# Optimization experiments

Measured on AMD Instinct MI355X. Metric: run time of the kernel, lower is better.

The kernel has to match this reference:

```python
import jax, jax.numpy as jnp
import numpy as np

B, N, D = 4, 2048, 1024
H = 16
HD = D // H


def setup_inputs() -> dict:
    key = jax.random.key(0)
    ks = jax.random.split(key, 7)
    bound_w = 1.0 / np.sqrt(D)  # kaiming_uniform(a=sqrt(5)) on (D, D) -> U(-1/sqrt(fan_in), 1/sqrt(fan_in))
    x = jax.random.normal(ks[0], (B, N, D), dtype=jnp.float32)
    Wq = jax.random.uniform(ks[1], (D, D), jnp.float32, -bound_w, bound_w)
    Wk = jax.random.uniform(ks[2], (D, D), jnp.float32, -bound_w, bound_w)
    Wv = jax.random.uniform(ks[3], (D, D), jnp.float32, -bound_w, bound_w)
    Wo = jax.random.uniform(ks[4], (D, D), jnp.float32, -bound_w, bound_w)
    bo = jax.random.uniform(ks[5], (D,), jnp.float32, -bound_w, bound_w)
    return {"x": x, "Wq": Wq, "Wk": Wk, "Wv": Wv, "Wo": Wo, "bo": bo}


def reference(x, Wq, Wk, Wv, Wo, bo):
    b, n, _ = x.shape
    # QKV projections: contraction over W's FIRST axis, matching torch einsum 'bnd,di->bni'
    Q = jnp.einsum('bnd,di->bni', x, Wq)
    K = jnp.einsum('bnd,di->bni', x, Wk)
    V = jnp.einsum('bnd,di->bni', x, Wv)
    # split heads: [b, h, n, hd]
    Q = Q.reshape(b, n, H, HD).transpose(0, 2, 1, 3)
    K = K.reshape(b, n, H, HD).transpose(0, 2, 1, 3)
    V = V.reshape(b, n, H, HD).transpose(0, 2, 1, 3)
    scores = jnp.einsum('bhnd,bhmd->bhnm', Q, K) / np.sqrt(HD).astype(np.float32)
    causal = jnp.triu(jnp.ones((n, n), dtype=bool), k=1)  # True above diagonal -> masked
    scores = jnp.where(causal[None, None, :, :], -jnp.inf, scores)
    attn = jax.nn.softmax(scores, axis=-1)
    # dropout rate is 0.0 -> identity
    ctx = jnp.einsum('bhnm,bhmd->bhnd', attn, V)
    ctx = ctx.transpose(0, 2, 1, 3).reshape(b, n, D)
    return ctx @ Wo.T + bo
```

## Files before the change

kernel.cpp:

```cpp
#include <hip/hip_runtime.h>
#include <hip/hip_bf16.h>

typedef __bf16 bf16;
typedef __bf16 bf16x4 __attribute__((ext_vector_type(4)));
typedef __bf16 bf16x8 __attribute__((ext_vector_type(8)));
typedef float  f32x4  __attribute__((ext_vector_type(4)));

#define B_  4
#define N_  2048
#define D_  1024
#define H_  16
#define HD_ 64

#define QSCALE 0.1803368801111204f

__device__ __forceinline__ bf16x8 ld8(const bf16* p) {
  return *reinterpret_cast<const bf16x8*>(p);
}
__device__ __forceinline__ float max3f(float a, float b, float c) {
  return fmaxf(fmaxf(a, b), c);
}

__device__ __forceinline__ void gload16(const bf16* g, bf16* l) {
  __builtin_amdgcn_global_load_lds(
      (const __attribute__((address_space(1))) void*)g,
      (__attribute__((address_space(3))) void*)l, 16, 0, 0);
}

__global__ __launch_bounds__(256) void cast_k(const float* __restrict__ in,
                                              bf16* __restrict__ out, int n) {
  int i = (blockIdx.x * 256 + threadIdx.x) * 8;
  if (i >= n) return;
  float4 a = *reinterpret_cast<const float4*>(in + i);
  float4 b = *reinterpret_cast<const float4*>(in + i + 4);
  bf16x8 o;
  o[0] = (bf16)a.x; o[1] = (bf16)a.y; o[2] = (bf16)a.z; o[3] = (bf16)a.w;
  o[4] = (bf16)b.x; o[5] = (bf16)b.y; o[6] = (bf16)b.z; o[7] = (bf16)b.w;
  *reinterpret_cast<bf16x8*>(out + i) = o;
}

__global__ __launch_bounds__(1024)
void transpose3_k(const float* __restrict__ w0, const float* __restrict__ w1,
                  const float* __restrict__ w2, bf16* __restrict__ out) {
  __shared__ float t[32][33];
  const int z = blockIdx.z;
  const float* in = (z == 0) ? w0 : (z == 1) ? w1 : w2;
  const float scale = (z == 0) ? QSCALE : 1.0f;
  bf16* o = out + (size_t)z * D_ * D_;
  int c = blockIdx.x * 32 + threadIdx.x;
  int r = blockIdx.y * 32 + threadIdx.y;
  t[threadIdx.y][threadIdx.x] = in[r * D_ + c];
  __syncthreads();
  int oc = blockIdx.y * 32 + threadIdx.x;
  int orr = blockIdx.x * 32 + threadIdx.y;
  o[orr * D_ + oc] = (bf16)(scale * t[threadIdx.x][threadIdx.y]);
}

#define GEMM_CORE(A_, Bt_, K_)                                                   \
  f32x4 acc[4][4] = {};                                                          \
  for (int kk = 0; kk < (K_); kk += 32) {                                        \
    _Pragma("unroll")                                                            \
    for (int j = 0; j < 2; ++j) {                                                \
      gload16(&(A_)[(size_t)(brow + wid * 32 + j * 16 + (lane >> 2)) * (K_) +    \
                    kk + (lane & 3) * 8],                                        \
              &As[(wid * 32 + j * 16) * 32]);                                    \
      gload16(&(Bt_)[(size_t)(bcol + wid * 32 + j * 16 + (lane >> 2)) * (K_) +   \
                     kk + (lane & 3) * 8],                                       \
              &Bs[(wid * 32 + j * 16) * 32]);                                    \
    }                                                                            \
    __syncthreads();                                                             \
    bf16x8 af[4], bfr[4];                                                        \
    _Pragma("unroll")                                                            \
    for (int m = 0; m < 4; ++m)                                                  \
      af[m] = *reinterpret_cast<const bf16x8*>(&As[(wr + m * 16 + l15) * 32 + lk]); \
    _Pragma("unroll")                                                            \
    for (int n = 0; n < 4; ++n)                                                  \
      bfr[n] = *reinterpret_cast<const bf16x8*>(&Bs[(wc + n * 16 + l15) * 32 + lk]); \
    _Pragma("unroll")                                                            \
    for (int m = 0; m < 4; ++m)                                                  \
      _Pragma("unroll")                                                          \
      for (int n = 0; n < 4; ++n)                                                \
        acc[m][n] = __builtin_amdgcn_mfma_f32_16x16x32_bf16(af[m], bfr[n],       \
                                                            acc[m][n], 0, 0, 0); \
    __syncthreads();                                                             \
  }

__global__ __launch_bounds__(256)
void gemm_qkv(const bf16* __restrict__ A, const bf16* __restrict__ Bt,
              bf16* __restrict__ qb, bf16* __restrict__ kb, bf16* __restrict__ vtb)
{
  __shared__ bf16 As[128 * 32];
  __shared__ bf16 Bs[128 * 32];
  const int tid  = threadIdx.x;
  const int lane = tid & 63;
  const int wid  = tid >> 6;
  const int wg   = blockIdx.x;
  const int xcd  = wg & 7;
  const int idx  = wg >> 3;
  const int brow = ((xcd << 3) + (idx & 7)) * 128;
  const int bcol = (idx >> 3) * 128;
  const int wr   = (wid >> 1) * 64;
  const int wc   = (wid & 1) * 64;
  const int l15  = lane & 15;
  const int lk   = (lane >> 4) * 8;

  GEMM_CORE(A, Bt, D_)

  const int which = bcol >> 10;
  bf16* outp = (which == 0) ? qb : (which == 1) ? kb : vtb;
  const int r0 = (lane >> 4) * 4;
#pragma unroll
  for (int m = 0; m < 4; ++m)
#pragma unroll
    for (int n = 0; n < 4; ++n)
#pragma unroll
      for (int r = 0; r < 4; ++r) {
        int grow = brow + wr + m * 16 + r0 + r;
        int gcol = (bcol & 1023) + wc + n * 16 + l15;
        int b = grow >> 11, nn = grow & (N_ - 1);
        int h = gcol >> 6, hd = gcol & 63;
        float v = acc[m][n][r];
        if (which == 2)
          outp[((size_t)((b * H_ + h) * HD_ + hd)) * N_ + nn] = (bf16)v;
        else
          outp[((((size_t)(b * H_ + h)) * N_ + nn) << 6) + hd] = (bf16)v;
      }
}

__global__ __launch_bounds__(256)
void gemm_out(const bf16* __restrict__ A, const bf16* __restrict__ Bt,
              float* __restrict__ C, const float* __restrict__ bias)
{
  __shared__ bf16 As[128 * 32];
  __shared__ bf16 Bs[128 * 32];
  const int tid  = threadIdx.x;
  const int lane = tid & 63;
  const int wid  = tid >> 6;
  const int wg   = blockIdx.x;
  const int xcd  = wg & 7;
  const int idx  = wg >> 3;
  const int brow = ((xcd << 3) + (idx & 7)) * 128;
  const int bcol = (idx >> 3) * 128;
  const int wr   = (wid >> 1) * 64;
  const int wc   = (wid & 1) * 64;
  const int l15  = lane & 15;
  const int lk   = (lane >> 4) * 8;

  GEMM_CORE(A, Bt, D_)

  const int r0 = (lane >> 4) * 4;
#pragma unroll
  for (int m = 0; m < 4; ++m)
#pragma unroll
    for (int n = 0; n < 4; ++n)
#pragma unroll
      for (int r = 0; r < 4; ++r) {
        int grow = brow + wr + m * 16 + r0 + r;
        int gcol = bcol + wc + n * 16 + l15;
        C[(size_t)grow * D_ + gcol] = acc[m][n][r] + bias[gcol];
      }
}

__global__ __launch_bounds__(512, 6)
void attn_k(const bf16* __restrict__ q, const bf16* __restrict__ k,
            const bf16* __restrict__ vt, bf16* __restrict__ ctx)
{
  __shared__ bf16 Ks[2][64 * 64];
  __shared__ bf16 Vs[2][64 * 64];
  __shared__ bf16 Pl[8][16][72];
  const int tid  = threadIdx.x;
  const int lane = tid & 63;
  const int wid  = tid >> 6;
  const int bid  = blockIdx.x;
  const int bh   = bid & 63;
  const int cpr  = bid >> 6;
  const int l15  = lane & 15;
  const int g    = lane >> 4;
  const int lk   = g * 8;
  const int swz  = (l15 & 7) << 4;

  const bf16* kp = k  + (size_t)bh * N_ * HD_;
  const bf16* vp = vt + (size_t)bh * HD_ * N_;
  const int b = bh >> 4, h = bh & 15;

  const int srow  = wid * 8 + (lane >> 3);
  const int scoff = ((lane & 7) ^ (srow & 7)) * 8;
  const int sdoff = wid * 8 * 64;

  bf16x8 ones8;
#pragma unroll
  for (int i = 0; i < 8; ++i) ones8[i] = (bf16)1.0f;

#pragma unroll
  for (int p = 0; p < 2; ++p) {
    const int qb0   = (p == 0 ? cpr : 15 - cpr) * 128;
    const int qbase = qb0 + wid * 16;
    const int nt    = qb0 / 64 + 2;
    const int tm    = qbase >> 6;

    const bf16* qp = q + ((size_t)bh * N_ + qbase) * HD_;
    bf16x8 aq[2];
#pragma unroll
    for (int c2 = 0; c2 < 2; ++c2)
      aq[c2] = ld8(qp + (size_t)l15 * HD_ + c2 * 32 + lk);

    float m_run = -1e30f;
    f32x4 oacc[5] = {};

    gload16(kp + (size_t)srow * HD_ + scoff, &Ks[0][sdoff]);
    gload16(vp + (size_t)srow * N_ + scoff, &Vs[0][sdoff]);
    __syncthreads();

    for (int t = 0; t < nt; ++t) {
      const int cur = t & 1;
      if (t + 1 < nt) {
        const int kb = (t + 1) * 64;
        gload16(kp + (size_t)(kb + srow) * HD_ + scoff, &Ks[cur ^ 1][sdoff]);
        gload16(vp + (size_t)srow * N_ + kb + scoff, &Vs[cur ^ 1][sdoff]);
      }
      if (t <= tm) {
        const char* kb_ = (const char*)&Ks[cur][0];
        const char* vb_ = (const char*)&Vs[cur][0];

        f32x4 s[4] = {};
#pragma unroll
        for (int tt = 0; tt < 4; ++tt) {
          bf16x8 bk0 = *reinterpret_cast<const bf16x8*>(
              kb_ + (tt * 16 + l15) * 128 + ((g * 16) ^ swz));
          bf16x8 bk1 = *reinterpret_cast<const bf16x8*>(
              kb_ + (tt * 16 + l15) * 128 + ((64 + g * 16) ^ swz));
          s[tt] = __builtin_amdgcn_mfma_f32_16x16x32_bf16(bk0, aq[0], s[tt], 0, 0, 0);
          s[tt] = __builtin_amdgcn_mfma_f32_16x16x32_bf16(bk1, aq[1], s[tt], 0, 0, 0);
        }

        if (t == tm) {
          const int qr = qbase + l15;
#pragma unroll
          for (int tt = 0; tt < 4; ++tt)
#pragma unroll
            for (int r = 0; r < 4; ++r) {
              int kq = t * 64 + tt * 16 + g * 4 + r;
              if (kq > qr) s[tt][r] = -1e30f;
            }
        }

        float pm = max3f(s[0][0], s[0][1], s[0][2]);
        pm = max3f(pm, s[0][3], s[1][0]);
        pm = max3f(pm, s[1][1], s[1][2]);
        pm = max3f(pm, s[1][3], s[2][0]);
        pm = max3f(pm, s[2][1], s[2][2]);
        pm = max3f(pm, s[2][3], s[3][0]);
        pm = max3f(pm, s[3][1], s[3][2]);
        pm = fmaxf(pm, s[3][3]);
        pm = fmaxf(pm, __shfl_xor(pm, 16));
        pm = fmaxf(pm, __shfl_xor(pm, 32));
        if (!__all(pm <= m_run + 8.f)) {
          float mn = fmaxf(m_run, pm);
          float al = exp2f(m_run - mn);
          m_run = mn;
#pragma unroll
          for (int n = 0; n < 5; ++n)
#pragma unroll
            for (int r = 0; r < 4; ++r) oacc[n][r] *= al;
        }
#pragma unroll
        for (int tt = 0; tt < 4; ++tt)
#pragma unroll
          for (int r = 0; r < 4; ++r) s[tt][r] = exp2f(s[tt][r] - m_run);

#pragma unroll
        for (int tt = 0; tt < 4; ++tt) {
          bf16x4 pk;
#pragma unroll
          for (int r = 0; r < 4; ++r) pk[r] = (bf16)s[tt][r];
          *reinterpret_cast<bf16x4*>(&Pl[wid][l15][tt * 16 + g * 4]) = pk;
        }

#pragma unroll
        for (int kc = 0; kc < 2; ++kc) {
          bf16x8 pb = *reinterpret_cast<const bf16x8*>(&Pl[wid][l15][kc * 32 + lk]);
#pragma unroll
          for (int n = 0; n < 4; ++n) {
            bf16x8 vf = *reinterpret_cast<const bf16x8*>(
                vb_ + (n * 16 + l15) * 128 + ((kc * 64 + g * 16) ^ swz));
            oacc[n] = __builtin_amdgcn_mfma_f32_16x16x32_bf16(vf, pb, oacc[n], 0, 0, 0);
          }
          oacc[4] = __builtin_amdgcn_mfma_f32_16x16x32_bf16(ones8, pb, oacc[4], 0, 0, 0);
        }
      }
      __syncthreads();
    }

    float inv = 1.f / oacc[4][0];
    bf16* cp = ctx + ((size_t)b * N_ + qbase + l15) * D_ + h * HD_;
#pragma unroll
    for (int n = 0; n < 4; ++n) {
      bf16x4 o;
#pragma unroll
      for (int r = 0; r < 4; ++r) o[r] = (bf16)(oacc[n][r] * inv);
      *reinterpret_cast<bf16x4*>(cp + n * 16 + g * 4) = o;
    }
  }
}

extern "C" void kernel_launch(void* const* d_in, const int* in_sizes, int n_in,
                              void* d_out, int out_size, void* d_ws, size_t ws_size,
                              hipStream_t stream)
{
  const float* x  = (const float*)d_in[0];
  const float* Wq = (const float*)d_in[1];
  const float* Wk = (const float*)d_in[2];
  const float* Wv = (const float*)d_in[3];
  const float* Wo = (const float*)d_in[4];
  const float* bo = (const float*)d_in[5];
  float* out = (float*)d_out;

  const size_t SZ_BHND = (size_t)B_ * H_ * N_ * HD_ * sizeof(bf16);
  const size_t SZ_W    = (size_t)D_ * D_ * sizeof(bf16);
  char* ws = (char*)d_ws;
  bf16* xbf  = (bf16*)(ws);
  bf16* ctx  = (bf16*)(ws);
  bf16* qb   = (bf16*)(ws + SZ_BHND);
  bf16* kbf  = (bf16*)(ws + 2 * SZ_BHND);
  bf16* vtb  = (bf16*)(ws + 3 * SZ_BHND);
  bf16* wqkv = (bf16*)(ws + 4 * SZ_BHND);
  bf16* wob  = (bf16*)(ws + 4 * SZ_BHND + 3 * SZ_W);
  if (ws_size < 4 * SZ_BHND + 4 * SZ_W) return;

  const int NX = B_ * N_ * D_;
  cast_k<<<NX / (256 * 8), 256, 0, stream>>>(x, xbf, NX);
  cast_k<<<(D_ * D_) / (256 * 8), 256, 0, stream>>>(Wo, wob, D_ * D_);

  transpose3_k<<<dim3(32, 32, 3), dim3(32, 32), 0, stream>>>(Wq, Wk, Wv, wqkv);

  gemm_qkv<<<1536, 256, 0, stream>>>(xbf, wqkv, qb, kbf, vtb);

  attn_k<<<512, 512, 0, stream>>>(qb, kbf, vtb, ctx);

  gemm_out<<<512, 256, 0, stream>>>(ctx, wob, out, bo);
}
```

Measured before the change: 195.1 us.

## Deepen GEMM K-tile with swizzled LDS; split attention into 64-row blocks

The GEMM core now stages 64-wide K tiles with an XOR-swizzled LDS layout, which halves the number of barriers and is meant to avoid LDS bank conflicts. The attention kernel drops the paired 128-row causal blocks of 8 waves and instead launches 2048 blocks of 4 waves, each handling 64 query rows, ordered longest-first. This removes the idle waves that skipped tiles past their diagonal and gives finer load balancing. In exchange, each K/V tile is reused by fewer waves, so K/V loads are amortized over less work, and LDS use per GEMM block doubles.

```diff
diff --git a/kernel.cpp b/kernel.cpp
--- a/kernel.cpp
+++ b/kernel.cpp
@@ -56,41 +56,47 @@
   o[orr * D_ + oc] = (bf16)(scale * t[threadIdx.x][threadIdx.y]);
 }
 
-#define GEMM_CORE(A_, Bt_, K_)                                                   \
-  f32x4 acc[4][4] = {};                                                          \
-  for (int kk = 0; kk < (K_); kk += 32) {                                        \
-    _Pragma("unroll")                                                            \
-    for (int j = 0; j < 2; ++j) {                                                \
-      gload16(&(A_)[(size_t)(brow + wid * 32 + j * 16 + (lane >> 2)) * (K_) +    \
-                    kk + (lane & 3) * 8],                                        \
-              &As[(wid * 32 + j * 16) * 32]);                                    \
-      gload16(&(Bt_)[(size_t)(bcol + wid * 32 + j * 16 + (lane >> 2)) * (K_) +   \
-                     kk + (lane & 3) * 8],                                       \
-              &Bs[(wid * 32 + j * 16) * 32]);                                    \
-    }                                                                            \
-    __syncthreads();                                                             \
-    bf16x8 af[4], bfr[4];                                                        \
-    _Pragma("unroll")                                                            \
-    for (int m = 0; m < 4; ++m)                                                  \
-      af[m] = *reinterpret_cast<const bf16x8*>(&As[(wr + m * 16 + l15) * 32 + lk]); \
-    _Pragma("unroll")                                                            \
-    for (int n = 0; n < 4; ++n)                                                  \
-      bfr[n] = *reinterpret_cast<const bf16x8*>(&Bs[(wc + n * 16 + l15) * 32 + lk]); \
-    _Pragma("unroll")                                                            \
-    for (int m = 0; m < 4; ++m)                                                  \
-      _Pragma("unroll")                                                          \
-      for (int n = 0; n < 4; ++n)                                                \
-        acc[m][n] = __builtin_amdgcn_mfma_f32_16x16x32_bf16(af[m], bfr[n],       \
-                                                            acc[m][n], 0, 0, 0); \
-    __syncthreads();                                                             \
+#define GEMM_CORE(A_, Bt_, K_)                                                    \
+  f32x4 acc[4][4] = {};                                                           \
+  const int sr8   = lane >> 3;                           \
+  const int schk  = ((lane & 7) ^ sr8) * 8;         \
+  const int swz7  = (l15 & 7);                                                    \
+  for (int kk = 0; kk < (K_); kk += 64) {                                         \
+    _Pragma("unroll")                                                             \
+    for (int j = 0; j < 4; ++j) {                                                 \
+      const int rr = j * 32 + wid * 8 + sr8;                                      \
+      gload16(&(A_)[(size_t)(brow + rr) * (K_) + kk + schk],                      \
+              &As[(j * 32 + wid * 8) * 64]);                                      \
+      gload16(&(Bt_)[(size_t)(bcol + rr) * (K_) + kk + schk],                     \
+              &Bs[(j * 32 + wid * 8) * 64]);                                      \
+    }                                                                             \
+    __syncthreads();                                                              \
+    _Pragma("unroll")                                                             \
+    for (int s = 0; s < 2; ++s) {                                                 \
+      const int q = ((s * 4 + g) ^ swz7) * 8;                                     \
+      bf16x8 af[4], bfr[4];                                                       \
+      _Pragma("unroll")                                                           \
+      for (int m = 0; m < 4; ++m)                                                 \
+        af[m] = *reinterpret_cast<const bf16x8*>(&As[(wr + m * 16 + l15) * 64 + q]); \
+      _Pragma("unroll")                                                           \
+      for (int n = 0; n < 4; ++n)                                                 \
+        bfr[n] = *reinterpret_cast<const bf16x8*>(&Bs[(wc + n * 16 + l15) * 64 + q]); \
+      _Pragma("unroll")                                                           \
+      for (int m = 0; m < 4; ++m)                                                 \
+        _Pragma("unroll")                                                         \
+        for (int n = 0; n < 4; ++n)                                               \
+          acc[m][n] = __builtin_amdgcn_mfma_f32_16x16x32_bf16(af[m], bfr[n],      \
+                                                              acc[m][n], 0, 0, 0);\
+    }                                                                             \
+    __syncthreads();                                                              \
   }
 
 __global__ __launch_bounds__(256)
 void gemm_qkv(const bf16* __restrict__ A, const bf16* __restrict__ Bt,
               bf16* __restrict__ qb, bf16* __restrict__ kb, bf16* __restrict__ vtb)
 {
-  __shared__ bf16 As[128 * 32];
-  __shared__ bf16 Bs[128 * 32];
+  __shared__ bf16 As[128 * 64];
+  __shared__ bf16 Bs[128 * 64];
   const int tid  = threadIdx.x;
   const int lane = tid & 63;
   const int wid  = tid >> 6;
@@ -102,13 +108,13 @@
   const int wr   = (wid >> 1) * 64;
   const int wc   = (wid & 1) * 64;
   const int l15  = lane & 15;
-  const int lk   = (lane >> 4) * 8;
+  const int g    = lane >> 4;
 
   GEMM_CORE(A, Bt, D_)
 
   const int which = bcol >> 10;
   bf16* outp = (which == 0) ? qb : (which == 1) ? kb : vtb;
-  const int r0 = (lane >> 4) * 4;
+  const int r0 = g * 4;
 #pragma unroll
   for (int m = 0; m < 4; ++m)
 #pragma unroll
@@ -131,8 +137,8 @@
 void gemm_out(const bf16* __restrict__ A, const bf16* __restrict__ Bt,
               float* __restrict__ C, const float* __restrict__ bias)
 {
-  __shared__ bf16 As[128 * 32];
-  __shared__ bf16 Bs[128 * 32];
+  __shared__ bf16 As[128 * 64];
+  __shared__ bf16 Bs[128 * 64];
   const int tid  = threadIdx.x;
   const int lane = tid & 63;
   const int wid  = tid >> 6;
@@ -144,11 +150,11 @@
   const int wr   = (wid >> 1) * 64;
   const int wc   = (wid & 1) * 64;
   const int l15  = lane & 15;
-  const int lk   = (lane >> 4) * 8;
+  const int g    = lane >> 4;
 
   GEMM_CORE(A, Bt, D_)
 
-  const int r0 = (lane >> 4) * 4;
+  const int r0 = g * 4;
 #pragma unroll
   for (int m = 0; m < 4; ++m)
 #pragma unroll
@@ -161,19 +167,19 @@
       }
 }
 
-__global__ __launch_bounds__(512, 6)
+__global__ __launch_bounds__(256, 3)
 void attn_k(const bf16* __restrict__ q, const bf16* __restrict__ k,
             const bf16* __restrict__ vt, bf16* __restrict__ ctx)
 {
   __shared__ bf16 Ks[2][64 * 64];
   __shared__ bf16 Vs[2][64 * 64];
-  __shared__ bf16 Pl[8][16][72];
+  __shared__ bf16 Pl[4][16][72];
   const int tid  = threadIdx.x;
   const int lane = tid & 63;
   const int wid  = tid >> 6;
   const int bid  = blockIdx.x;
   const int bh   = bid & 63;
-  const int cpr  = bid >> 6;
+  const int c    = 31 - (bid >> 6);
   const int l15  = lane & 15;
   const int g    = lane >> 4;
   const int lk   = g * 8;
@@ -183,123 +189,127 @@
   const bf16* vp = vt + (size_t)bh * HD_ * N_;
   const int b = bh >> 4, h = bh & 15;
 
-  const int srow  = wid * 8 + (lane >> 3);
-  const int scoff = ((lane & 7) ^ (srow & 7)) * 8;
-  const int sdoff = wid * 8 * 64;
+  const int sr8   = lane >> 3;
+  const int scoff = ((lane & 7) ^ sr8) * 8;
 
   bf16x8 ones8;
 #pragma unroll
   for (int i = 0; i < 8; ++i) ones8[i] = (bf16)1.0f;
 
-#pragma unroll
-  for (int p = 0; p < 2; ++p) {
-    const int qb0   = (p == 0 ? cpr : 15 - cpr) * 128;
-    const int qbase = qb0 + wid * 16;
-    const int nt    = qb0 / 64 + 2;
-    const int tm    = qbase >> 6;
-
-    const bf16* qp = q + ((size_t)bh * N_ + qbase) * HD_;
-    bf16x8 aq[2];
-#pragma unroll
-    for (int c2 = 0; c2 < 2; ++c2)
-      aq[c2] = ld8(qp + (size_t)l15 * HD_ + c2 * 32 + lk);
-
-    float m_run = -1e30f;
-    f32x4 oacc[5] = {};
-
-    gload16(kp + (size_t)srow * HD_ + scoff, &Ks[0][sdoff]);
-    gload16(vp + (size_t)srow * N_ + scoff, &Vs[0][sdoff]);
+  const int qbase = c * 64 + wid * 16;
+  const int nt    = c + 1;
+
+  const bf16* qp = q + ((size_t)bh * N_ + qbase) * HD_;
+  bf16x8 aq[2];
+#pragma unroll
+  for (int c2 = 0; c2 < 2; ++c2)
+    aq[c2] = ld8(qp + (size_t)l15 * HD_ + c2 * 32 + lk);
+
+  float m_run = -1e30f;
+  f32x4 oacc[5] = {};
+
+#pragma unroll
+  for (int j = 0; j < 2; ++j) {
+    const int rr = j * 32 + wid * 8 + sr8;
+    gload16(kp + (size_t)rr * HD_ + scoff, &Ks[0][(j * 32 + wid * 8) * 64]);
+    gload16(vp + (size_t)rr * N_ + scoff, &Vs[0][(j * 32 + wid * 8) * 64]);
+  }
+  __syncthreads();
+
+  for (int t = 0; t < nt; ++t) {
+    const int cur = t & 1;
+    if (t + 1 < nt) {
+      const int kb = (t + 1) * 64;
+#pragma unroll
+      for (int j = 0; j < 2; ++j) {
+        const int rr = j * 32 + wid * 8 + sr8;
+        gload16(kp + (size_t)(kb + rr) * HD_ + scoff,
+                &Ks[cur ^ 1][(j * 32 + wid * 8) * 64]);
+        gload16(vp + (size_t)rr * N_ + kb + scoff,
+                &Vs[cur ^ 1][(j * 32 + wid * 8) * 64]);
+      }
+    }
+    {
+      const char* kb_ = (const char*)&Ks[cur][0];
+      const char* vb_ = (const char*)&Vs[cur][0];
+
+      f32x4 s[4] = {};
+#pragma unroll
+      for (int tt = 0; tt < 4; ++tt) {
+        bf16x8 bk0 = *reinterpret_cast<const bf16x8*>(
+            kb_ + (tt * 16 + l15) * 128 + ((g * 16) ^ swz));
+        bf16x8 bk1 = *reinterpret_cast<const bf16x8*>(
+            kb_ + (tt * 16 + l15) * 128 + ((64 + g * 16) ^ swz));
+        s[tt] = __builtin_amdgcn_mfma_f32_16x16x32_bf16(bk0, aq[0], s[tt], 0, 0, 0);
+        s[tt] = __builtin_amdgcn_mfma_f32_16x16x32_bf16(bk1, aq[1], s[tt], 0, 0, 0);
+      }
+
+      if (t == nt - 1) {
+        const int qr = qbase + l15;
+#pragma unroll
+        for (int tt = 0; tt < 4; ++tt)
+#pragma unroll
+          for (int r = 0; r < 4; ++r) {
+            int kq = t * 64 + tt * 16 + g * 4 + r;
+            if (kq > qr) s[tt][r] = -1e30f;
+          }
+      }
+
+      float pm = max3f(s[0][0], s[0][1], s[0][2]);
+      pm = max3f(pm, s[0][3], s[1][0]);
+      pm = max3f(pm, s[1][1], s[1][2]);
+      pm = max3f(pm, s[1][3], s[2][0]);
+      pm = max3f(pm, s[2][1], s[2][2]);
+      pm = max3f(pm, s[2][3], s[3][0]);
+      pm = max3f(pm, s[3][1], s[3][2]);
+      pm = fmaxf(pm, s[3][3]);
+      pm = fmaxf(pm, __shfl_xor(pm, 16));
+      pm = fmaxf(pm, __shfl_xor(pm, 32));
+      if (!__all(pm <= m_run + 8.f)) {
+        float mn = fmaxf(m_run, pm);
+        float al = exp2f(m_run - mn);
+        m_run = mn;
+#pragma unroll
+        for (int n = 0; n < 5; ++n)
+#pragma unroll
+          for (int r = 0; r < 4; ++r) oacc[n][r] *= al;
+      }
+#pragma unroll
+      for (int tt = 0; tt < 4; ++tt)
+#pragma unroll
+        for (int r = 0; r < 4; ++r) s[tt][r] = exp2f(s[tt][r] - m_run);
+
+#pragma unroll
+      for (int tt = 0; tt < 4; ++tt) {
+        bf16x4 pk;
+#pragma unroll
+        for (int r = 0; r < 4; ++r) pk[r] = (bf16)s[tt][r];
+        *reinterpret_cast<bf16x4*>(&Pl[wid][l15][tt * 16 + g * 4]) = pk;
+      }
+
+#pragma unroll
+      for (int kc = 0; kc < 2; ++kc) {
+        bf16x8 pb = *reinterpret_cast<const bf16x8*>(&Pl[wid][l15][kc * 32 + lk]);
+#pragma unroll
+        for (int n = 0; n < 4; ++n) {
+          bf16x8 vf = *reinterpret_cast<const bf16x8*>(
+              vb_ + (n * 16 + l15) * 128 + ((kc * 64 + g * 16) ^ swz));
+          oacc[n] = __builtin_amdgcn_mfma_f32_16x16x32_bf16(vf, pb, oacc[n], 0, 0, 0);
+        }
+        oacc[4] = __builtin_amdgcn_mfma_f32_16x16x32_bf16(ones8, pb, oacc[4], 0, 0, 0);
+      }
+    }
     __syncthreads();
-
-    for (int t = 0; t < nt; ++t) {
-      const int cur = t & 1;
-      if (t + 1 < nt) {
-        const int kb = (t + 1) * 64;
-        gload16(kp + (size_t)(kb + srow) * HD_ + scoff, &Ks[cur ^ 1][sdoff]);
-        gload16(vp + (size_t)srow * N_ + kb + scoff, &Vs[cur ^ 1][sdoff]);
-      }
-      if (t <= tm) {
-        const char* kb_ = (const char*)&Ks[cur][0];
-        const char* vb_ = (const char*)&Vs[cur][0];
-
-        f32x4 s[4] = {};
-#pragma unroll
-        for (int tt = 0; tt < 4; ++tt) {
-          bf16x8 bk0 = *reinterpret_cast<const bf16x8*>(
-              kb_ + (tt * 16 + l15) * 128 + ((g * 16) ^ swz));
-          bf16x8 bk1 = *reinterpret_cast<const bf16x8*>(
-              kb_ + (tt * 16 + l15) * 128 + ((64 + g * 16) ^ swz));
-          s[tt] = __builtin_amdgcn_mfma_f32_16x16x32_bf16(bk0, aq[0], s[tt], 0, 0, 0);
-          s[tt] = __builtin_amdgcn_mfma_f32_16x16x32_bf16(bk1, aq[1], s[tt], 0, 0, 0);
-        }
-
-        if (t == tm) {
-          const int qr = qbase + l15;
-#pragma unroll
-          for (int tt = 0; tt < 4; ++tt)
-#pragma unroll
-            for (int r = 0; r < 4; ++r) {
-              int kq = t * 64 + tt * 16 + g * 4 + r;
-              if (kq > qr) s[tt][r] = -1e30f;
-            }
-        }
-
-        float pm = max3f(s[0][0], s[0][1], s[0][2]);
-        pm = max3f(pm, s[0][3], s[1][0]);
-        pm = max3f(pm, s[1][1], s[1][2]);
-        pm = max3f(pm, s[1][3], s[2][0]);
-        pm = max3f(pm, s[2][1], s[2][2]);
-        pm = max3f(pm, s[2][3], s[3][0]);
-        pm = max3f(pm, s[3][1], s[3][2]);
-        pm = fmaxf(pm, s[3][3]);
-        pm = fmaxf(pm, __shfl_xor(pm, 16));
-        pm = fmaxf(pm, __shfl_xor(pm, 32));
-        if (!__all(pm <= m_run + 8.f)) {
-          float mn = fmaxf(m_run, pm);
-          float al = exp2f(m_run - mn);
-          m_run = mn;
-#pragma unroll
-          for (int n = 0; n < 5; ++n)
-#pragma unroll
-            for (int r = 0; r < 4; ++r) oacc[n][r] *= al;
-        }
-#pragma unroll
-        for (int tt = 0; tt < 4; ++tt)
-#pragma unroll
-          for (int r = 0; r < 4; ++r) s[tt][r] = exp2f(s[tt][r] - m_run);
-
-#pragma unroll
-        for (int tt = 0; tt < 4; ++tt) {
-          bf16x4 pk;
-#pragma unroll
-          for (int r = 0; r < 4; ++r) pk[r] = (bf16)s[tt][r];
-          *reinterpret_cast<bf16x4*>(&Pl[wid][l15][tt * 16 + g * 4]) = pk;
-        }
-
-#pragma unroll
-        for (int kc = 0; kc < 2; ++kc) {
-          bf16x8 pb = *reinterpret_cast<const bf16x8*>(&Pl[wid][l15][kc * 32 + lk]);
-#pragma unroll
-          for (int n = 0; n < 4; ++n) {
-            bf16x8 vf = *reinterpret_cast<const bf16x8*>(
-                vb_ + (n * 16 + l15) * 128 + ((kc * 64 + g * 16) ^ swz));
-            oacc[n] = __builtin_amdgcn_mfma_f32_16x16x32_bf16(vf, pb, oacc[n], 0, 0, 0);
-          }
-          oacc[4] = __builtin_amdgcn_mfma_f32_16x16x32_bf16(ones8, pb, oacc[4], 0, 0, 0);
-        }
-      }
-      __syncthreads();
-    }
-
-    float inv = 1.f / oacc[4][0];
-    bf16* cp = ctx + ((size_t)b * N_ + qbase + l15) * D_ + h * HD_;
-#pragma unroll
-    for (int n = 0; n < 4; ++n) {
-      bf16x4 o;
-#pragma unroll
-      for (int r = 0; r < 4; ++r) o[r] = (bf16)(oacc[n][r] * inv);
-      *reinterpret_cast<bf16x4*>(cp + n * 16 + g * 4) = o;
-    }
+  }
+
+  float inv = 1.f / oacc[4][0];
+  bf16* cp = ctx + ((size_t)b * N_ + qbase + l15) * D_ + h * HD_;
+#pragma unroll
+  for (int n = 0; n < 4; ++n) {
+    bf16x4 o;
+#pragma unroll
+    for (int r = 0; r < 4; ++r) o[r] = (bf16)(oacc[n][r] * inv);
+    *reinterpret_cast<bf16x4*>(cp + n * 16 + g * 4) = o;
   }
 }
 
@@ -335,7 +345,7 @@
 
   gemm_qkv<<<1536, 256, 0, stream>>>(xbf, wqkv, qb, kbf, vtb);
 
-  attn_k<<<512, 512, 0, stream>>>(qb, kbf, vtb, ctx);
+  attn_k<<<2048, 256, 0, stream>>>(qb, kbf, vtb, ctx);
 
   gemm_out<<<512, 256, 0, stream>>>(ctx, wob, out, bo);
 }
```

Result: no change. 196.4 us (+0.7%).
